# Optimization experiments

Measured on AMD Instinct MI355X. Metric: run time of the kernel, lower is better.

Reference implementation:

```python
import jax, jax.numpy as jnp
import numpy as np
import math

DIM = 1024
N_HEADS = 16
HEAD_DIM = DIM // N_HEADS
FFN_HIDDEN = 4096
EPS = 1e-6


def setup_inputs() -> dict:
    key = jax.random.key(0)
    ks = jax.random.split(key, 10)
    s = 1.0 / math.sqrt(DIM)
    sh = 1.0 / math.sqrt(FFN_HIDDEN)
    return {
        "x": jax.random.normal(ks[0], (2, 2048, DIM), dtype=jnp.float32),
        # attention weights stored as [in, out] (y = x @ W)
        "wq": jax.random.normal(ks[1], (DIM, DIM), dtype=jnp.float32) * s,
        "wk": jax.random.normal(ks[2], (DIM, DIM), dtype=jnp.float32) * s,
        "wv": jax.random.normal(ks[3], (DIM, DIM), dtype=jnp.float32) * s,
        "wo": jax.random.normal(ks[4], (DIM, DIM), dtype=jnp.float32) * s,
        "w_gate": jax.random.normal(ks[5], (DIM, FFN_HIDDEN), dtype=jnp.float32) * s,
        "w_up": jax.random.normal(ks[6], (DIM, FFN_HIDDEN), dtype=jnp.float32) * s,
        "w_down": jax.random.normal(ks[7], (FFN_HIDDEN, DIM), dtype=jnp.float32) * sh,
        "attn_norm_w": jnp.ones((DIM,), dtype=jnp.float32),
        "ffn_norm_w": jnp.ones((DIM,), dtype=jnp.float32),
    }


def rmsnorm(x, w):
    xf = x.astype(jnp.float32)
    rms = jax.lax.rsqrt(jnp.mean(xf * xf, axis=-1, keepdims=True) + EPS)
    return (xf * rms).astype(x.dtype) * w


def attention(x, wq, wk, wv, wo):
    B, T, C = x.shape
    q = (x @ wq).reshape(B, T, N_HEADS, HEAD_DIM)
    k = (x @ wk).reshape(B, T, N_HEADS, HEAD_DIM)
    v = (x @ wv).reshape(B, T, N_HEADS, HEAD_DIM)
    scores = jnp.einsum("bqhd,bkhd->bhqk", q, k) / math.sqrt(HEAD_DIM)
    causal = jnp.tril(jnp.ones((T, T), dtype=bool))  # True = keep
    scores = jnp.where(causal, scores, -jnp.inf)
    attn = jax.nn.softmax(scores, axis=-1)
    out = jnp.einsum("bhqk,bkhd->bqhd", attn, v).reshape(B, T, C)
    return out @ wo


def swiglu(x, w_gate, w_up, w_down):
    return (jax.nn.silu(x @ w_gate) * (x @ w_up)) @ w_down


def reference(x, wq, wk, wv, wo, w_gate, w_up, w_down, attn_norm_w, ffn_norm_w):
    x = x + attention(rmsnorm(x, attn_norm_w), wq, wk, wv, wo)
    x = x + swiglu(rmsnorm(x, ffn_norm_w), w_gate, w_up, w_down)
    return x
```

## Files before the change

kernel.cpp:

```cpp
#include <hip/hip_runtime.h>
#include <hip/hip_bf16.h>
#include <stdint.h>
#include <math.h>

#define DIM   1024
#define TSEQ  2048
#define BATCH 2
#define NH    16
#define HD    64
#define FFN   4096
#define ROWS  (BATCH*TSEQ)
#define QKVN  (3*DIM)

typedef __attribute__((ext_vector_type(8))) short s16x8;
typedef __attribute__((ext_vector_type(4))) float f32x4;

__device__ __forceinline__ unsigned short f2bf(float f) {
  union { float f; unsigned u; } v; v.f = f;
  unsigned r = v.u + 0x7fffu + ((v.u >> 16) & 1u);
  return (unsigned short)(r >> 16);
}
__device__ __forceinline__ float bf2f(unsigned short h) {
  union { unsigned u; float f; } v; v.u = ((unsigned)h) << 16; return v.f;
}
__device__ __forceinline__ unsigned pack_bf2(float lo, float hi) {
  union { float f; unsigned u; } a, c; a.f = lo; c.f = hi;
  return (c.u & 0xffff0000u) | (a.u >> 16);
}

__device__ __forceinline__ void gld16(const void* g, void* l) {
  __builtin_amdgcn_global_load_lds((const __attribute__((address_space(1))) void*)g,
                                   (__attribute__((address_space(3))) void*)l, 16, 0, 0);
}

__device__ __forceinline__ int xcd_swz_flat() {
  const int nx = gridDim.x, ny = gridDim.y;
  const int nwg = nx * ny * gridDim.z;
  const int flat = blockIdx.x + nx * (blockIdx.y + ny * blockIdx.z);
  return (flat & 7) * (nwg >> 3) + (flat >> 3);
}

__global__ void wtrans_k(const float* __restrict__ w, unsigned short* __restrict__ wt,
                         int K, int N, int mode)
{
  __shared__ unsigned short t[64][65];
  const int n0 = blockIdx.x * 64, k0 = blockIdx.y * 64;
  const int tid = threadIdx.x;
  #pragma unroll
  for (int i = 0; i < 16; ++i) {
    const int r = i*4 + (tid >> 6), c = tid & 63;
    t[r][c] = f2bf(w[(size_t)(k0 + r) * N + n0 + c]);
  }
  __syncthreads();
  #pragma unroll
  for (int i = 0; i < 16; ++i) {
    const int r = i*4 + (tid >> 6), c = tid & 63;
    const int n = n0 + r;
    int dr = n;
    if (mode == 1) dr = ((n >> 4) << 5) + (n & 15);
    if (mode == 2) dr = ((n >> 4) << 5) + 16 + (n & 15);
    wt[(size_t)dr * K + k0 + c] = t[c][r];
  }
}

__global__ void vtrans_k(const unsigned short* __restrict__ qkv, unsigned short* __restrict__ vt)
{
  __shared__ unsigned short t[64][65];
  const int tt0 = blockIdx.x * 64;
  const int bh = blockIdx.y, b = bh >> 4, h = bh & 15;
  const int tid = threadIdx.x;
  const unsigned short* src = qkv + (size_t)(b*TSEQ + tt0) * QKVN + 2*DIM + h*HD;
  #pragma unroll
  for (int i = 0; i < 16; ++i) {
    const int r = i*4 + (tid >> 6), c = tid & 63;
    t[r][c] = src[(size_t)r * QKVN + c];
  }
  __syncthreads();
  unsigned short* dst = vt + (size_t)bh * HD * TSEQ + tt0;
  #pragma unroll
  for (int i = 0; i < 16; ++i) {
    const int d = i*4 + (tid >> 6), c = tid & 63;
    dst[(size_t)d * TSEQ + c] = t[c][d];
  }
}

__global__ void rmsnorm_k(const float* __restrict__ x, const float* __restrict__ w,
                          unsigned short* __restrict__ o)
{
  const int row = blockIdx.x, tid = threadIdx.x;
  const float4 v = ((const float4*)(x + (size_t)row * DIM))[tid];
  float ss = v.x*v.x + v.y*v.y + v.z*v.z + v.w*v.w;
  #pragma unroll
  for (int off = 32; off >= 1; off >>= 1) ss += __shfl_xor(ss, off);
  __shared__ float sred[4];
  if ((tid & 63) == 0) sred[tid >> 6] = ss;
  __syncthreads();
  const float tot = sred[0] + sred[1] + sred[2] + sred[3];
  const float r = rsqrtf(tot * (1.0f/DIM) + 1e-6f);
  const float4 wv = ((const float4*)w)[tid];
  ushort4 ov;
  ov.x = f2bf(v.x*r*wv.x); ov.y = f2bf(v.y*r*wv.y);
  ov.z = f2bf(v.z*r*wv.z); ov.w = f2bf(v.w*r*wv.w);
  ((ushort4*)(o + (size_t)row * DIM))[tid] = ov;
}

__global__ void rmsnorm3_k(const float* __restrict__ x, const float* __restrict__ p0,
                           const float* __restrict__ p1, const float* __restrict__ w,
                           float* __restrict__ x1, unsigned short* __restrict__ o)
{
  const int row = blockIdx.x, tid = threadIdx.x;
  const size_t base = (size_t)row * DIM;
  const float4 a = ((const float4*)(x + base))[tid];
  const float4 b = ((const float4*)(p0 + base))[tid];
  const float4 c = ((const float4*)(p1 + base))[tid];
  float4 v;
  v.x = a.x + b.x + c.x; v.y = a.y + b.y + c.y;
  v.z = a.z + b.z + c.z; v.w = a.w + b.w + c.w;
  ((float4*)(x1 + base))[tid] = v;
  float ss = v.x*v.x + v.y*v.y + v.z*v.z + v.w*v.w;
  #pragma unroll
  for (int off = 32; off >= 1; off >>= 1) ss += __shfl_xor(ss, off);
  __shared__ float sred[4];
  if ((tid & 63) == 0) sred[tid >> 6] = ss;
  __syncthreads();
  const float tot = sred[0] + sred[1] + sred[2] + sred[3];
  const float r = rsqrtf(tot * (1.0f/DIM) + 1e-6f);
  const float4 wv = ((const float4*)w)[tid];
  ushort4 ov;
  ov.x = f2bf(v.x*r*wv.x); ov.y = f2bf(v.y*r*wv.y);
  ov.z = f2bf(v.z*r*wv.z); ov.w = f2bf(v.w*r*wv.w);
  ((ushort4*)(o + base))[tid] = ov;
}

__global__ void resadd3_k(const float* __restrict__ x1, const float* __restrict__ q0,
                          const float* __restrict__ q1, float* __restrict__ o)
{
  const size_t i = (size_t)blockIdx.x * 256 + threadIdx.x;
  const float4 a = ((const float4*)x1)[i];
  const float4 b = ((const float4*)q0)[i];
  const float4 c = ((const float4*)q1)[i];
  float4 v;
  v.x = a.x + b.x + c.x; v.y = a.y + b.y + c.y;
  v.z = a.z + b.z + c.z; v.w = a.w + b.w + c.w;
  ((float4*)o)[i] = v;
}

__global__ void gemm128sp(const unsigned short* __restrict__ A, int lda,
                          const unsigned short* __restrict__ BT, int ldb,
                          float* __restrict__ P, int ldc, int Khalf)
{
  __shared__ __align__(16) unsigned short lA[128*64];
  __shared__ __align__(16) unsigned short lB[128*64];
  const int nx = gridDim.x, ny = gridDim.y;
  const int w = xcd_swz_flat();
  const int bx = w % nx, by = (w / nx) % ny, bz = w / (nx * ny);
  const int tid = threadIdx.x;
  const int lane = tid & 63;
  const int wid = tid >> 6;
  const int m0 = by * 128, n0 = bx * 128;
  const int Koff = bz * Khalf;
  P += (size_t)bz * ((size_t)ny * 128) * ldc;
  const int wr = (wid >> 1) * 64, wc = (wid & 1) * 64;
  const int lrow = lane & 15, lk8 = (lane >> 4) * 8;

  f32x4 acc[4][4] = {};

  for (int k0 = Koff; k0 < Koff + Khalf; k0 += 64) {
    #pragma unroll
    for (int c = 0; c < 4; ++c) {
      const int boff = c*4096 + tid*16;
      const int row = boff >> 7, colb = boff & 127;
      gld16((const char*)A + ((size_t)(m0+row)*lda + k0)*2 + colb, (char*)lA + boff);
    }
    #pragma unroll
    for (int c = 0; c < 4; ++c) {
      const int boff = c*4096 + tid*16;
      const int row = boff >> 7, colb = boff & 127;
      gld16((const char*)BT + ((size_t)(n0+row)*ldb + k0)*2 + colb, (char*)lB + boff);
    }
    __syncthreads();
    #pragma unroll
    for (int kk = 0; kk < 64; kk += 32) {
      s16x8 af[4], bf[4];
      #pragma unroll
      for (int i = 0; i < 4; ++i) af[i] = *(const s16x8*)&lA[(wr + i*16 + lrow)*64 + kk + lk8];
      #pragma unroll
      for (int j = 0; j < 4; ++j) bf[j] = *(const s16x8*)&lB[(wc + j*16 + lrow)*64 + kk + lk8];
      #pragma unroll
      for (int i = 0; i < 4; ++i)
        #pragma unroll
        for (int j = 0; j < 4; ++j)
          acc[i][j] = __builtin_amdgcn_mfma_f32_16x16x32_bf16(af[i], bf[j], acc[i][j], 0, 0, 0);
    }
    __syncthreads();
  }
  const int er = (lane >> 4) * 4, ec = lane & 15;
  #pragma unroll
  for (int i = 0; i < 4; ++i)
    #pragma unroll
    for (int j = 0; j < 4; ++j) {
      const int gr = m0 + wr + i*16 + er;
      const int gc = n0 + wc + j*16 + ec;
      #pragma unroll
      for (int e = 0; e < 4; ++e)
        P[(size_t)(gr + e) * ldc + gc] = acc[i][j][e];
    }
}

template<int EPI>
__global__ __launch_bounds__(512) void gemm256(const unsigned short* __restrict__ A, int lda,
                                               const unsigned short* __restrict__ BT, int ldb,
                                               void* __restrict__ Cout, int ldc, int K)
{
  __shared__ __align__(16) unsigned short lA[2][256*64];
  __shared__ __align__(16) unsigned short lB[2][256*64];
  const int nx = gridDim.x;
  const int wsz = xcd_swz_flat();
  const int bx = wsz % nx, by = wsz / nx;
  const int tid = threadIdx.x, lane = tid & 63, wid = tid >> 6;
  const int lrow = lane & 15, g = lane >> 4;
  const int wm = wid >> 2, wn = wid & 3;
  const int m0 = by * 256, n0 = bx * 256;

  const int r0 = tid >> 3;
  const int eB = ((r0 >> 5) << 6) | (r0 & 31);
  const int lc0 = ((tid & 7) * 16) ^ ((r0 & 7) << 4);
  const char* pA = (const char*)A + ((size_t)(m0 + r0) * lda) * 2 + lc0;
  const char* pB = (const char*)BT + ((size_t)(n0 + eB) * ldb) * 2 + lc0;
  char* dA = (char*)&lA[0][0] + tid * 16;
  char* dB = (char*)&lB[0][0] + eB * 128 + (tid & 7) * 16;
  const size_t a64 = (size_t)64 * lda * 2;
  const size_t b32 = (size_t)32 * ldb * 2;

#define STG_GA0(t) do { const char* s_ = pA + (size_t)(t) * 128; \
    char* d_ = dA + (((t) & 1) * 32768); \
    gld16(s_, d_); gld16(s_ + 2*a64, d_ + 16384); } while (0)
#define STG_GA1(t) do { const char* s_ = pA + (size_t)(t) * 128 + a64; \
    char* d_ = dA + (((t) & 1) * 32768) + 8192; \
    gld16(s_, d_); gld16(s_ + 2*a64, d_ + 16384); } while (0)
#define STG_GB0(t) do { const char* s_ = pB + (size_t)(t) * 128; \
    char* d_ = dB + (((t) & 1) * 32768); \
    gld16(s_, d_); gld16(s_ + 4*b32, d_ + 16384); } while (0)
#define STG_GB1(t) do { const char* s_ = pB + (size_t)(t) * 128 + b32; \
    char* d_ = dB + (((t) & 1) * 32768) + 4096; \
    gld16(s_, d_); gld16(s_ + 4*b32, d_ + 16384); } while (0)

  const int swz = (lrow & 7) << 4;
  const int c0 = (g * 16) ^ swz;
  const int c1 = c0 ^ 64;
  const char* rdA = (const char*)&lA[0][0] + (wm * 128 + lrow) * 128;
  const char* rdB = (const char*)&lB[0][0] + (wn * 64 + lrow) * 128;

  f32x4 acc[8][4] = {};
  s16x8 a0[4][2], a1[4][2], b0[2][2], b1[2][2];

#define MFMA_Q(rh, ch, AF, BF) do { \
    _Pragma("unroll") \
    for (int i_ = 0; i_ < 4; ++i_) { \
      _Pragma("unroll") \
      for (int j_ = 0; j_ < 2; ++j_) { \
        acc[(rh)*4+i_][(ch)*2+j_] = __builtin_amdgcn_mfma_f32_16x16x32_bf16(AF[i_][0], BF[j_][0], acc[(rh)*4+i_][(ch)*2+j_], 0,0,0); \
        acc[(rh)*4+i_][(ch)*2+j_] = __builtin_amdgcn_mfma_f32_16x16x32_bf16(AF[i_][1], BF[j_][1], acc[(rh)*4+i_][(ch)*2+j_], 0,0,0); \
      } } } while (0)

  const int NT = K >> 6;

  STG_GA0(0); STG_GB0(0); STG_GB1(0); STG_GA1(0);
  asm volatile("s_waitcnt vmcnt(4)" ::: "memory");
  __builtin_amdgcn_s_barrier();

  for (int t = 0; t < NT; ++t) {
    const char* bufA = rdA + (t & 1) * 32768;
    const char* bufB = rdB + (t & 1) * 32768;
    const bool more = (t + 1 < NT);
    #pragma unroll
    for (int i = 0; i < 4; ++i) {
      a0[i][0] = *(const s16x8*)(bufA + i*2048 + c0);
      a0[i][1] = *(const s16x8*)(bufA + i*2048 + c1);
    }
    #pragma unroll
    for (int j = 0; j < 2; ++j) {
      b0[j][0] = *(const s16x8*)(bufB + j*2048 + c0);
      b0[j][1] = *(const s16x8*)(bufB + j*2048 + c1);
    }
    if (more) { STG_GA0(t + 1); STG_GB0(t + 1); }
    __builtin_amdgcn_s_barrier();
    asm volatile("s_waitcnt lgkmcnt(0)" ::: "memory");
    __builtin_amdgcn_sched_barrier(0);
    __builtin_amdgcn_s_setprio(1);
    MFMA_Q(0, 0, a0, b0);
    __builtin_amdgcn_s_setprio(0);
    if (more) { asm volatile("s_waitcnt vmcnt(6)" ::: "memory"); }
    else      { asm volatile("s_waitcnt vmcnt(2)" ::: "memory"); }
    __builtin_amdgcn_s_barrier();
    #pragma unroll
    for (int j = 0; j < 2; ++j) {
      b1[j][0] = *(const s16x8*)(bufB + 4096 + j*2048 + c0);
      b1[j][1] = *(const s16x8*)(bufB + 4096 + j*2048 + c1);
    }
    if (more) STG_GB1(t + 1);
    __builtin_amdgcn_s_barrier();
    asm volatile("s_waitcnt lgkmcnt(0)" ::: "memory");
    __builtin_amdgcn_sched_barrier(0);
    __builtin_amdgcn_s_setprio(1);
    MFMA_Q(0, 1, a0, b1);
    __builtin_amdgcn_s_setprio(0);
    if (more) { asm volatile("s_waitcnt vmcnt(6)" ::: "memory"); }
    else      { asm volatile("s_waitcnt vmcnt(0)" ::: "memory"); }
    __builtin_amdgcn_s_barrier();
    #pragma unroll
    for (int i = 0; i < 4; ++i) {
      a1[i][0] = *(const s16x8*)(bufA + 8192 + i*2048 + c0);
      a1[i][1] = *(const s16x8*)(bufA + 8192 + i*2048 + c1);
    }
    if (more) STG_GA1(t + 1);
    __builtin_amdgcn_s_barrier();
    asm volatile("s_waitcnt lgkmcnt(0)" ::: "memory");
    __builtin_amdgcn_sched_barrier(0);
    __builtin_amdgcn_s_setprio(1);
    MFMA_Q(1, 1, a1, b1);
    __builtin_amdgcn_s_setprio(0);
    __builtin_amdgcn_s_barrier();
    __builtin_amdgcn_s_setprio(1);
    MFMA_Q(1, 0, a1, b0);
    __builtin_amdgcn_s_setprio(0);
    if (more) { asm volatile("s_waitcnt vmcnt(4)" ::: "memory"); }
    __builtin_amdgcn_s_barrier();
  }

  const int er = g * 4, ec = lane & 15;
  if (EPI == 0) {
    unsigned short* C = (unsigned short*)Cout;
    #pragma unroll
    for (int i = 0; i < 8; ++i)
      #pragma unroll
      for (int j = 0; j < 4; ++j) {
        const int gr = m0 + wm*128 + i*16 + er;
        const int gc = n0 + wn*64 + j*16 + ec;
        #pragma unroll
        for (int e = 0; e < 4; ++e)
          C[(size_t)(gr + e) * ldc + gc] = f2bf(acc[i][j][e]);
      }
  } else {
    unsigned short* C = (unsigned short*)Cout;
    #pragma unroll
    for (int i = 0; i < 8; ++i)
      #pragma unroll
      for (int tp = 0; tp < 2; ++tp) {
        const int gr = m0 + wm*128 + i*16 + er;
        const int hc = (n0 >> 1) + wn*32 + tp*16 + ec;
        #pragma unroll
        for (int e = 0; e < 4; ++e) {
          const float gv = acc[i][2*tp][e];
          const float uv = acc[i][2*tp + 1][e];
          const float hv = gv / (1.f + __expf(-gv)) * uv;
          C[(size_t)(gr + e) * ldc + hc] = f2bf(hv);
        }
      }
  }
#undef STG_GA0
#undef STG_GA1
#undef STG_GB0
#undef STG_GB1
#undef MFMA_Q
}

__global__ __launch_bounds__(512) void attn_fwd(const unsigned short* __restrict__ qkv,
                                                const unsigned short* __restrict__ vt,
                                                unsigned short* __restrict__ outp)
{
  __shared__ __align__(16) unsigned short lK[2][64*64];
  __shared__ __align__(16) unsigned short lV[2][64*64];
  const int nx = gridDim.x;
  const int wsz = xcd_swz_flat();
  const int qblk = wsz % nx;
  const int bh = wsz / nx, b = bh >> 4, h = bh & 15;
  const int tid = threadIdx.x, wid = tid >> 6, lane = tid & 63;
  const int lq = lane & 15, g = lane >> 4;

  const int qrow = qblk*128 + wid*16;
  const int myq = qrow + lq;

  const size_t qbase = ((size_t)(b*TSEQ + myq)) * QKVN + h*HD;
  const s16x8 qf0 = *(const s16x8*)&qkv[qbase + g*8];
  const s16x8 qf1 = *(const s16x8*)&qkv[qbase + 32 + g*8];

  const int boff = tid * 16;
  const int loff = boff ^ (((boff >> 7) & 7) << 4);
  const int srow = loff >> 7;
  const int scolb = loff & 127;
  const char* ksrc0 = (const char*)qkv +
      (((size_t)(b*TSEQ + srow)) * QKVN + DIM + h*HD) * 2 + scolb;
  const char* vsrc0 = (const char*)vt +
      (((size_t)bh*HD + srow) * TSEQ) * 2 + scolb;

  float mrun = -INFINITY, lrun = 0.f;
  f32x4 of[4] = {};

  const int nkt = 2*qblk + 2;

  gld16(ksrc0, (char*)lK[0] + boff);
  gld16(vsrc0, (char*)lV[0] + boff);
  int cur = 0;

  for (int kt = 0; kt < nkt; ++kt) {
    __syncthreads();
    if (kt + 1 < nkt) {
      gld16(ksrc0 + (size_t)(kt+1)*64*(QKVN*2), (char*)lK[cur^1] + boff);
      gld16(vsrc0 + (size_t)(kt+1)*128,         (char*)lV[cur^1] + boff);
    }
    if (kt*64 <= qrow + 15) {
      const unsigned short* Kb = lK[cur];
      const unsigned short* Vb = lV[cur];
      f32x4 sacc[4] = {};
      #pragma unroll
      for (int s = 0; s < 4; ++s) {
        const int r = s*16 + lq;
        const int sw = (r & 7) << 4;
        const s16x8 kf0 = *(const s16x8*)((const char*)Kb + r*128 + ((g*16) ^ sw));
        const s16x8 kf1 = *(const s16x8*)((const char*)Kb + r*128 + ((64 + g*16) ^ sw));
        sacc[s] = __builtin_amdgcn_mfma_f32_16x16x32_bf16(kf0, qf0, sacc[s], 0,0,0);
        sacc[s] = __builtin_amdgcn_mfma_f32_16x16x32_bf16(kf1, qf1, sacc[s], 0,0,0);
      }
      float p[4][4];
      float mt = -INFINITY;
      #pragma unroll
      for (int s = 0; s < 4; ++s)
        #pragma unroll
        for (int e = 0; e < 4; ++e) {
          const int key = kt*64 + s*16 + 4*g + e;
          const float v = (key <= myq) ? sacc[s][e]*0.125f : -INFINITY;
          p[s][e] = v;
          mt = fmaxf(mt, v);
        }
      mt = fmaxf(mt, __shfl_xor(mt, 16));
      mt = fmaxf(mt, __shfl_xor(mt, 32));
      const float mnew = fmaxf(mrun, mt);
      const float scale = __expf(mrun - mnew);
      float ssum = 0.f;
      #pragma unroll
      for (int s = 0; s < 4; ++s)
        #pragma unroll
        for (int e = 0; e < 4; ++e) {
          p[s][e] = __expf(p[s][e] - mnew);
          ssum += p[s][e];
        }
      ssum += __shfl_xor(ssum, 16);
      ssum += __shfl_xor(ssum, 32);
      lrun = lrun * scale + ssum;
      mrun = mnew;
      #pragma unroll
      for (int d0b = 0; d0b < 4; ++d0b) of[d0b] = of[d0b] * scale;
      #pragma unroll
      for (int hh = 0; hh < 2; ++hh) {
        unsigned w[4];
        #pragma unroll
        for (int j = 0; j < 4; ++j) w[j] = pack_bf2(p[2*hh][j], p[2*hh+1][j]);
        s16x8 bp;
        #pragma unroll
        for (int e = 0; e < 8; ++e) {
          const int srcg = 2*(g & 1) + (e >> 2);
          const unsigned ww = (unsigned)__shfl((int)w[e & 3], lq | (srcg << 4));
          bp[e] = (short)((g >= 2) ? (ww >> 16) : (ww & 0xffffu));
        }
        #pragma unroll
        for (int d0b = 0; d0b < 4; ++d0b) {
          const int r = d0b*16 + lq;
          const int sw = (r & 7) << 4;
          const s16x8 vf = *(const s16x8*)((const char*)Vb + r*128 + ((hh*64 + g*16) ^ sw));
          of[d0b] = __builtin_amdgcn_mfma_f32_16x16x32_bf16(vf, bp, of[d0b], 0,0,0);
        }
      }
    }
    cur ^= 1;
  }
  const float inv = 1.f / lrun;
  const size_t obase = ((size_t)(b*TSEQ + myq)) * DIM + h*HD;
  #pragma unroll
  for (int d0b = 0; d0b < 4; ++d0b) {
    ushort4 o;
    o.x = f2bf(of[d0b][0] * inv);
    o.y = f2bf(of[d0b][1] * inv);
    o.z = f2bf(of[d0b][2] * inv);
    o.w = f2bf(of[d0b][3] * inv);
    *(ushort4*)&outp[obase + d0b*16 + 4*g] = o;
  }
}

extern "C" void kernel_launch(void* const* d_in, const int* in_sizes, int n_in,
                              void* d_out, int out_size, void* d_ws, size_t ws_size,
                              hipStream_t stream)
{
  const float* x   = (const float*)d_in[0];
  const float* wq  = (const float*)d_in[1];
  const float* wk  = (const float*)d_in[2];
  const float* wv  = (const float*)d_in[3];
  const float* wo  = (const float*)d_in[4];
  const float* wg  = (const float*)d_in[5];
  const float* wu  = (const float*)d_in[6];
  const float* wd  = (const float*)d_in[7];
  const float* anw = (const float*)d_in[8];
  const float* fnw = (const float*)d_in[9];
  float* outp = (float*)d_out;

  const size_t MB = 1024*1024;
  char* ws = (char*)d_ws;
  float*          x1    = (float*)         (ws + 0);
  unsigned short* wdT   = (unsigned short*)(ws + 16*MB);
  unsigned short* wguT  = (unsigned short*)(ws + 24*MB);
  unsigned short* wqkvT = (unsigned short*)(ws + 40*MB);
  unsigned short* woT   = (unsigned short*)(ws + 46*MB);
  unsigned short* xn    = (unsigned short*)(ws + 48*MB);
  unsigned short* qkv   = (unsigned short*)(ws + 56*MB);
  unsigned short* vtb   = (unsigned short*)(ws + 80*MB);
  unsigned short* aout  = (unsigned short*)(ws + 88*MB);
  float*          pwo   = (float*)         (ws + 56*MB);
  unsigned short* hbuf  = (unsigned short*)(ws + 56*MB);
  float*          pdn   = (float*)         (ws + 24*MB);

  const dim3 blk(256);

  wtrans_k<<<dim3(16,16), blk, 0, stream>>>(wq, wqkvT,               DIM, DIM, 0);
  wtrans_k<<<dim3(16,16), blk, 0, stream>>>(wk, wqkvT + 1024*1024,   DIM, DIM, 0);
  wtrans_k<<<dim3(16,16), blk, 0, stream>>>(wv, wqkvT + 2*1024*1024, DIM, DIM, 0);
  wtrans_k<<<dim3(16,16), blk, 0, stream>>>(wo, woT,                 DIM, DIM, 0);
  wtrans_k<<<dim3(64,16), blk, 0, stream>>>(wg, wguT,                DIM, FFN, 1);
  wtrans_k<<<dim3(64,16), blk, 0, stream>>>(wu, wguT,                DIM, FFN, 2);
  wtrans_k<<<dim3(16,64), blk, 0, stream>>>(wd, wdT,                 FFN, DIM, 0);

  rmsnorm_k<<<ROWS, blk, 0, stream>>>(x, anw, xn);
  gemm256<0><<<dim3(QKVN/256, ROWS/256), dim3(512), 0, stream>>>(xn, DIM, wqkvT, DIM, qkv, QKVN, DIM);
  vtrans_k<<<dim3(TSEQ/64, BATCH*NH), blk, 0, stream>>>(qkv, vtb);
  attn_fwd<<<dim3(TSEQ/128, BATCH*NH), dim3(512), 0, stream>>>(qkv, vtb, aout);
  gemm128sp<<<dim3(DIM/128, ROWS/128, 2), blk, 0, stream>>>(aout, DIM, woT, DIM, pwo, DIM, DIM/2);
  rmsnorm3_k<<<ROWS, blk, 0, stream>>>(x, pwo, pwo + (size_t)ROWS*DIM, fnw, x1, xn);

  gemm256<2><<<dim3(2*FFN/256, ROWS/256), dim3(512), 0, stream>>>(xn, DIM, wguT, DIM, hbuf, FFN, DIM);
  gemm128sp<<<dim3(DIM/128, ROWS/128, 2), blk, 0, stream>>>(hbuf, FFN, wdT, FFN, pdn, DIM, FFN/2);
  resadd3_k<<<dim3(ROWS*DIM/1024), blk, 0, stream>>>(x1, pdn, pdn + (size_t)ROWS*DIM, outp);
}
```

Before: 321.7 us.

## Peel last GEMM iteration, reorder prefetch before LDS reads, merge QKV transposes

The gemm256 main loop is restructured so the final k-tile is peeled out, which removes the per-iteration `more` branches. Global prefetch stores are now issued before the LDS fragment reads, and several barriers are dropped (the ones that came before lgkmcnt waits). Separately, the three Q/K/V weight transpose launches are merged into one 3D-grid kernel to cut launch overhead. The reduced barrier set risks LDS write/read hazards if the double-buffer waits are not sufficient.

```diff
diff --git a/kernel.cpp b/kernel.cpp
--- a/kernel.cpp
+++ b/kernel.cpp
@@ -60,6 +60,27 @@
     if (mode == 1) dr = ((n >> 4) << 5) + (n & 15);
     if (mode == 2) dr = ((n >> 4) << 5) + 16 + (n & 15);
     wt[(size_t)dr * K + k0 + c] = t[c][r];
+  }
+}
+
+__global__ void wtrans_qkv_k(const float* __restrict__ wq, const float* __restrict__ wk,
+                             const float* __restrict__ wv, unsigned short* __restrict__ wt)
+{
+  __shared__ unsigned short t[64][65];
+  const int n0 = blockIdx.x * 64, k0 = blockIdx.y * 64, z = blockIdx.z;
+  const float* w = (z == 0) ? wq : (z == 1) ? wk : wv;
+  unsigned short* dst = wt + (size_t)z * DIM * DIM;
+  const int tid = threadIdx.x;
+  #pragma unroll
+  for (int i = 0; i < 16; ++i) {
+    const int r = i*4 + (tid >> 6), c = tid & 63;
+    t[r][c] = f2bf(w[(size_t)(k0 + r) * DIM + n0 + c]);
+  }
+  __syncthreads();
+  #pragma unroll
+  for (int i = 0; i < 16; ++i) {
+    const int r = i*4 + (tid >> 6), c = tid & 63;
+    dst[(size_t)(n0 + r) * DIM + k0 + c] = t[c][r];
   }
 }
 
@@ -263,69 +284,71 @@
         acc[(rh)*4+i_][(ch)*2+j_] = __builtin_amdgcn_mfma_f32_16x16x32_bf16(AF[i_][1], BF[j_][1], acc[(rh)*4+i_][(ch)*2+j_], 0,0,0); \
       } } } while (0)
 
+#define VMCNT(n) asm volatile("s_waitcnt vmcnt(" #n ")" ::: "memory")
+#define LGKM0()  do { asm volatile("s_waitcnt lgkmcnt(0)" ::: "memory"); \
+                      __builtin_amdgcn_sched_barrier(0); } while (0)
+#define BARRIER() do { __builtin_amdgcn_s_barrier(); \
+                       __builtin_amdgcn_sched_barrier(0); } while (0)
+
+#define DS_A0(buf) do { _Pragma("unroll") for (int i_ = 0; i_ < 4; ++i_) { \
+    a0[i_][0] = *(const s16x8*)((buf) + i_*2048 + c0); \
+    a0[i_][1] = *(const s16x8*)((buf) + i_*2048 + c1); } } while (0)
+#define DS_A1(buf) do { _Pragma("unroll") for (int i_ = 0; i_ < 4; ++i_) { \
+    a1[i_][0] = *(const s16x8*)((buf) + 8192 + i_*2048 + c0); \
+    a1[i_][1] = *(const s16x8*)((buf) + 8192 + i_*2048 + c1); } } while (0)
+#define DS_B0(buf) do { _Pragma("unroll") for (int j_ = 0; j_ < 2; ++j_) { \
+    b0[j_][0] = *(const s16x8*)((buf) + j_*2048 + c0); \
+    b0[j_][1] = *(const s16x8*)((buf) + j_*2048 + c1); } } while (0)
+#define DS_B1(buf) do { _Pragma("unroll") for (int j_ = 0; j_ < 2; ++j_) { \
+    b1[j_][0] = *(const s16x8*)((buf) + 4096 + j_*2048 + c0); \
+    b1[j_][1] = *(const s16x8*)((buf) + 4096 + j_*2048 + c1); } } while (0)
+
+#define PRIO_MFMA(rh, ch, AF, BF) do { \
+    __builtin_amdgcn_s_setprio(1); MFMA_Q(rh, ch, AF, BF); \
+    __builtin_amdgcn_s_setprio(0); } while (0)
+
   const int NT = K >> 6;
 
   STG_GA0(0); STG_GB0(0); STG_GB1(0); STG_GA1(0);
-  asm volatile("s_waitcnt vmcnt(4)" ::: "memory");
-  __builtin_amdgcn_s_barrier();
-
-  for (int t = 0; t < NT; ++t) {
+  VMCNT(4);
+  BARRIER();
+
+  for (int t = 0; t < NT - 1; ++t) {
     const char* bufA = rdA + (t & 1) * 32768;
     const char* bufB = rdB + (t & 1) * 32768;
-    const bool more = (t + 1 < NT);
-    #pragma unroll
-    for (int i = 0; i < 4; ++i) {
-      a0[i][0] = *(const s16x8*)(bufA + i*2048 + c0);
-      a0[i][1] = *(const s16x8*)(bufA + i*2048 + c1);
-    }
-    #pragma unroll
-    for (int j = 0; j < 2; ++j) {
-      b0[j][0] = *(const s16x8*)(bufB + j*2048 + c0);
-      b0[j][1] = *(const s16x8*)(bufB + j*2048 + c1);
-    }
-    if (more) { STG_GA0(t + 1); STG_GB0(t + 1); }
-    __builtin_amdgcn_s_barrier();
-    asm volatile("s_waitcnt lgkmcnt(0)" ::: "memory");
-    __builtin_amdgcn_sched_barrier(0);
-    __builtin_amdgcn_s_setprio(1);
-    MFMA_Q(0, 0, a0, b0);
-    __builtin_amdgcn_s_setprio(0);
-    if (more) { asm volatile("s_waitcnt vmcnt(6)" ::: "memory"); }
-    else      { asm volatile("s_waitcnt vmcnt(2)" ::: "memory"); }
-    __builtin_amdgcn_s_barrier();
-    #pragma unroll
-    for (int j = 0; j < 2; ++j) {
-      b1[j][0] = *(const s16x8*)(bufB + 4096 + j*2048 + c0);
-      b1[j][1] = *(const s16x8*)(bufB + 4096 + j*2048 + c1);
-    }
-    if (more) STG_GB1(t + 1);
-    __builtin_amdgcn_s_barrier();
-    asm volatile("s_waitcnt lgkmcnt(0)" ::: "memory");
-    __builtin_amdgcn_sched_barrier(0);
-    __builtin_amdgcn_s_setprio(1);
-    MFMA_Q(0, 1, a0, b1);
-    __builtin_amdgcn_s_setprio(0);
-    if (more) { asm volatile("s_waitcnt vmcnt(6)" ::: "memory"); }
-    else      { asm volatile("s_waitcnt vmcnt(0)" ::: "memory"); }
-    __builtin_amdgcn_s_barrier();
-    #pragma unroll
-    for (int i = 0; i < 4; ++i) {
-      a1[i][0] = *(const s16x8*)(bufA + 8192 + i*2048 + c0);
-      a1[i][1] = *(const s16x8*)(bufA + 8192 + i*2048 + c1);
-    }
-    if (more) STG_GA1(t + 1);
-    __builtin_amdgcn_s_barrier();
-    asm volatile("s_waitcnt lgkmcnt(0)" ::: "memory");
-    __builtin_amdgcn_sched_barrier(0);
-    __builtin_amdgcn_s_setprio(1);
-    MFMA_Q(1, 1, a1, b1);
-    __builtin_amdgcn_s_setprio(0);
-    __builtin_amdgcn_s_barrier();
-    __builtin_amdgcn_s_setprio(1);
-    MFMA_Q(1, 0, a1, b0);
-    __builtin_amdgcn_s_setprio(0);
-    if (more) { asm volatile("s_waitcnt vmcnt(4)" ::: "memory"); }
-    __builtin_amdgcn_s_barrier();
+    STG_GA0(t + 1); STG_GB0(t + 1);
+    DS_A0(bufA); DS_B0(bufB);
+    LGKM0();
+    PRIO_MFMA(0, 0, a0, b0);
+    VMCNT(6); BARRIER();
+    STG_GB1(t + 1);
+    DS_B1(bufB);
+    LGKM0();
+    PRIO_MFMA(0, 1, a0, b1);
+    VMCNT(6); BARRIER();
+    STG_GA1(t + 1);
+    DS_A1(bufA);
+    LGKM0();
+    PRIO_MFMA(1, 1, a1, b1);
+    BARRIER();
+    PRIO_MFMA(1, 0, a1, b0);
+    VMCNT(4); BARRIER();
+  }
+  {
+    const char* bufA = rdA + ((NT - 1) & 1) * 32768;
+    const char* bufB = rdB + ((NT - 1) & 1) * 32768;
+    DS_A0(bufA); DS_B0(bufB);
+    LGKM0();
+    PRIO_MFMA(0, 0, a0, b0);
+    VMCNT(2); BARRIER();
+    DS_B1(bufB);
+    LGKM0();
+    PRIO_MFMA(0, 1, a0, b1);
+    VMCNT(0); BARRIER();
+    DS_A1(bufA);
+    LGKM0();
+    PRIO_MFMA(1, 1, a1, b1);
+    PRIO_MFMA(1, 0, a1, b0);
   }
 
   const int er = g * 4, ec = lane & 15;
@@ -363,6 +386,14 @@
 #undef STG_GB0
 #undef STG_GB1
 #undef MFMA_Q
+#undef VMCNT
+#undef LGKM0
+#undef BARRIER
+#undef DS_A0
+#undef DS_A1
+#undef DS_B0
+#undef DS_B1
+#undef PRIO_MFMA
 }
 
 __global__ __launch_bounds__(512) void attn_fwd(const unsigned short* __restrict__ qkv,
@@ -520,13 +551,11 @@
 
   const dim3 blk(256);
 
-  wtrans_k<<<dim3(16,16), blk, 0, stream>>>(wq, wqkvT,               DIM, DIM, 0);
-  wtrans_k<<<dim3(16,16), blk, 0, stream>>>(wk, wqkvT + 1024*1024,   DIM, DIM, 0);
-  wtrans_k<<<dim3(16,16), blk, 0, stream>>>(wv, wqkvT + 2*1024*1024, DIM, DIM, 0);
-  wtrans_k<<<dim3(16,16), blk, 0, stream>>>(wo, woT,                 DIM, DIM, 0);
-  wtrans_k<<<dim3(64,16), blk, 0, stream>>>(wg, wguT,                DIM, FFN, 1);
-  wtrans_k<<<dim3(64,16), blk, 0, stream>>>(wu, wguT,                DIM, FFN, 2);
-  wtrans_k<<<dim3(16,64), blk, 0, stream>>>(wd, wdT,                 FFN, DIM, 0);
+  wtrans_qkv_k<<<dim3(16,16,3), blk, 0, stream>>>(wq, wk, wv, wqkvT);
+  wtrans_k<<<dim3(16,16), blk, 0, stream>>>(wo, woT, DIM, DIM, 0);
+  wtrans_k<<<dim3(64,16), blk, 0, stream>>>(wg, wguT, DIM, FFN, 1);
+  wtrans_k<<<dim3(64,16), blk, 0, stream>>>(wu, wguT, DIM, FFN, 2);
+  wtrans_k<<<dim3(16,64), blk, 0, stream>>>(wd, wdT, FFN, DIM, 0);
 
   rmsnorm_k<<<ROWS, blk, 0, stream>>>(x, anw, xn);
   gemm256<0><<<dim3(QKVN/256, ROWS/256), dim3(512), 0, stream>>>(xn, DIM, wqkvT, DIM, qkv, QKVN, DIM);
```

Result: slower. 347.6 us (+8.1%).

## Store split-K partials in bf16, split down-proj 4-way, and cluster GEMM tiles per XCD

Applied to the files above, without the earlier changes.

The split-K GEMM partial outputs are now written as bf16 instead of fp32, which halves partial-sum write and read traffic in the residual and norm kernels. The down projection is split four ways along K instead of two, for more parallelism, and the final residual kernel sums four partials. gemm256 maps tiles to XCDs as rectangular clusters to improve L2 reuse, and the three QKV weight transposes are merged into one launch. Rounding the partials to bf16 adds numerical error to the residual stream.

```diff
diff --git a/kernel.cpp b/kernel.cpp
--- a/kernel.cpp
+++ b/kernel.cpp
@@ -60,6 +60,27 @@
     if (mode == 1) dr = ((n >> 4) << 5) + (n & 15);
     if (mode == 2) dr = ((n >> 4) << 5) + 16 + (n & 15);
     wt[(size_t)dr * K + k0 + c] = t[c][r];
+  }
+}
+
+__global__ void wtrans_qkv_k(const float* __restrict__ wq, const float* __restrict__ wk,
+                             const float* __restrict__ wv, unsigned short* __restrict__ wt)
+{
+  __shared__ unsigned short t[64][65];
+  const int n0 = blockIdx.x * 64, k0 = blockIdx.y * 64, z = blockIdx.z;
+  const float* w = (z == 0) ? wq : (z == 1) ? wk : wv;
+  unsigned short* dst = wt + (size_t)z * DIM * DIM;
+  const int tid = threadIdx.x;
+  #pragma unroll
+  for (int i = 0; i < 16; ++i) {
+    const int r = i*4 + (tid >> 6), c = tid & 63;
+    t[r][c] = f2bf(w[(size_t)(k0 + r) * DIM + n0 + c]);
+  }
+  __syncthreads();
+  #pragma unroll
+  for (int i = 0; i < 16; ++i) {
+    const int r = i*4 + (tid >> 6), c = tid & 63;
+    dst[(size_t)(n0 + r) * DIM + k0 + c] = t[c][r];
   }
 }
 
@@ -104,18 +125,18 @@
   ((ushort4*)(o + (size_t)row * DIM))[tid] = ov;
 }
 
-__global__ void rmsnorm3_k(const float* __restrict__ x, const float* __restrict__ p0,
-                           const float* __restrict__ p1, const float* __restrict__ w,
+__global__ void rmsnorm3_k(const float* __restrict__ x, const unsigned short* __restrict__ p0,
+                           const unsigned short* __restrict__ p1, const float* __restrict__ w,
                            float* __restrict__ x1, unsigned short* __restrict__ o)
 {
   const int row = blockIdx.x, tid = threadIdx.x;
   const size_t base = (size_t)row * DIM;
   const float4 a = ((const float4*)(x + base))[tid];
-  const float4 b = ((const float4*)(p0 + base))[tid];
-  const float4 c = ((const float4*)(p1 + base))[tid];
+  const ushort4 b = ((const ushort4*)(p0 + base))[tid];
+  const ushort4 c = ((const ushort4*)(p1 + base))[tid];
   float4 v;
-  v.x = a.x + b.x + c.x; v.y = a.y + b.y + c.y;
-  v.z = a.z + b.z + c.z; v.w = a.w + b.w + c.w;
+  v.x = a.x + bf2f(b.x) + bf2f(c.x); v.y = a.y + bf2f(b.y) + bf2f(c.y);
+  v.z = a.z + bf2f(b.z) + bf2f(c.z); v.w = a.w + bf2f(b.w) + bf2f(c.w);
   ((float4*)(x1 + base))[tid] = v;
   float ss = v.x*v.x + v.y*v.y + v.z*v.z + v.w*v.w;
   #pragma unroll
@@ -132,22 +153,29 @@
   ((ushort4*)(o + base))[tid] = ov;
 }
 
-__global__ void resadd3_k(const float* __restrict__ x1, const float* __restrict__ q0,
-                          const float* __restrict__ q1, float* __restrict__ o)
+__global__ void resadd5_k(const float* __restrict__ x1,
+                          const unsigned short* __restrict__ q0, const unsigned short* __restrict__ q1,
+                          const unsigned short* __restrict__ q2, const unsigned short* __restrict__ q3,
+                          float* __restrict__ o)
 {
   const size_t i = (size_t)blockIdx.x * 256 + threadIdx.x;
   const float4 a = ((const float4*)x1)[i];
-  const float4 b = ((const float4*)q0)[i];
-  const float4 c = ((const float4*)q1)[i];
+  const ushort4 b = ((const ushort4*)q0)[i];
+  const ushort4 c = ((const ushort4*)q1)[i];
+  const ushort4 d = ((const ushort4*)q2)[i];
+  const ushort4 e = ((const ushort4*)q3)[i];
   float4 v;
-  v.x = a.x + b.x + c.x; v.y = a.y + b.y + c.y;
-  v.z = a.z + b.z + c.z; v.w = a.w + b.w + c.w;
+  v.x = a.x + bf2f(b.x) + bf2f(c.x) + bf2f(d.x) + bf2f(e.x);
+  v.y = a.y + bf2f(b.y) + bf2f(c.y) + bf2f(d.y) + bf2f(e.y);
+  v.z = a.z + bf2f(b.z) + bf2f(c.z) + bf2f(d.z) + bf2f(e.z);
+  v.w = a.w + bf2f(b.w) + bf2f(c.w) + bf2f(d.w) + bf2f(e.w);
   ((float4*)o)[i] = v;
 }
 
+template<int NS>
 __global__ void gemm128sp(const unsigned short* __restrict__ A, int lda,
                           const unsigned short* __restrict__ BT, int ldb,
-                          float* __restrict__ P, int ldc, int Khalf)
+                          unsigned short* __restrict__ P, int ldc, int Ksp)
 {
   __shared__ __align__(16) unsigned short lA[128*64];
   __shared__ __align__(16) unsigned short lB[128*64];
@@ -158,14 +186,14 @@
   const int lane = tid & 63;
   const int wid = tid >> 6;
   const int m0 = by * 128, n0 = bx * 128;
-  const int Koff = bz * Khalf;
+  const int Koff = bz * Ksp;
   P += (size_t)bz * ((size_t)ny * 128) * ldc;
   const int wr = (wid >> 1) * 64, wc = (wid & 1) * 64;
   const int lrow = lane & 15, lk8 = (lane >> 4) * 8;
 
   f32x4 acc[4][4] = {};
 
-  for (int k0 = Koff; k0 < Koff + Khalf; k0 += 64) {
+  for (int k0 = Koff; k0 < Koff + Ksp; k0 += 64) {
     #pragma unroll
     for (int c = 0; c < 4; ++c) {
       const int boff = c*4096 + tid*16;
@@ -203,20 +231,25 @@
       const int gc = n0 + wc + j*16 + ec;
       #pragma unroll
       for (int e = 0; e < 4; ++e)
-        P[(size_t)(gr + e) * ldc + gc] = acc[i][j][e];
+        P[(size_t)(gr + e) * ldc + gc] = f2bf(acc[i][j][e]);
     }
 }
 
 template<int EPI>
 __global__ __launch_bounds__(512) void gemm256(const unsigned short* __restrict__ A, int lda,
                                                const unsigned short* __restrict__ BT, int ldb,
-                                               void* __restrict__ Cout, int ldc, int K)
+                                               void* __restrict__ Cout, int ldc, int K,
+                                               int CX, int CY)
 {
   __shared__ __align__(16) unsigned short lA[2][256*64];
   __shared__ __align__(16) unsigned short lB[2][256*64];
-  const int nx = gridDim.x;
-  const int wsz = xcd_swz_flat();
-  const int bx = wsz % nx, by = wsz / nx;
+  const int nx = gridDim.x, ny = gridDim.y;
+  const int flat = blockIdx.x + nx * blockIdx.y;
+  const int xcd = flat & 7, k = flat >> 3;
+  const int RX = nx / CX, RY = ny / CY;
+  const int cx = xcd % CX, cy = xcd / CX;
+  const int bx = cx * RX + k % RX;
+  const int by = cy * RY + k / RX;
   const int tid = threadIdx.x, lane = tid & 63, wid = tid >> 6;
   const int lrow = lane & 15, g = lane >> 4;
   const int wm = wid >> 2, wn = wid & 3;
@@ -504,6 +537,7 @@
   float* outp = (float*)d_out;
 
   const size_t MB = 1024*1024;
+  const size_t RD = (size_t)ROWS * DIM;
   char* ws = (char*)d_ws;
   float*          x1    = (float*)         (ws + 0);
   unsigned short* wdT   = (unsigned short*)(ws + 16*MB);
@@ -514,28 +548,26 @@
   unsigned short* qkv   = (unsigned short*)(ws + 56*MB);
   unsigned short* vtb   = (unsigned short*)(ws + 80*MB);
   unsigned short* aout  = (unsigned short*)(ws + 88*MB);
-  float*          pwo   = (float*)         (ws + 56*MB);
+  unsigned short* pwo   = (unsigned short*)(ws + 56*MB);
   unsigned short* hbuf  = (unsigned short*)(ws + 56*MB);
-  float*          pdn   = (float*)         (ws + 24*MB);
+  unsigned short* pdn   = (unsigned short*)(ws + 24*MB);
 
   const dim3 blk(256);
 
-  wtrans_k<<<dim3(16,16), blk, 0, stream>>>(wq, wqkvT,               DIM, DIM, 0);
-  wtrans_k<<<dim3(16,16), blk, 0, stream>>>(wk, wqkvT + 1024*1024,   DIM, DIM, 0);
-  wtrans_k<<<dim3(16,16), blk, 0, stream>>>(wv, wqkvT + 2*1024*1024, DIM, DIM, 0);
-  wtrans_k<<<dim3(16,16), blk, 0, stream>>>(wo, woT,                 DIM, DIM, 0);
-  wtrans_k<<<dim3(64,16), blk, 0, stream>>>(wg, wguT,                DIM, FFN, 1);
-  wtrans_k<<<dim3(64,16), blk, 0, stream>>>(wu, wguT,                DIM, FFN, 2);
-  wtrans_k<<<dim3(16,64), blk, 0, stream>>>(wd, wdT,                 FFN, DIM, 0);
+  wtrans_qkv_k<<<dim3(16,16,3), blk, 0, stream>>>(wq, wk, wv, wqkvT);
+  wtrans_k<<<dim3(16,16), blk, 0, stream>>>(wo, woT, DIM, DIM, 0);
+  wtrans_k<<<dim3(64,16), blk, 0, stream>>>(wg, wguT, DIM, FFN, 1);
+  wtrans_k<<<dim3(64,16), blk, 0, stream>>>(wu, wguT, DIM, FFN, 2);
+  wtrans_k<<<dim3(16,64), blk, 0, stream>>>(wd, wdT, FFN, DIM, 0);
 
   rmsnorm_k<<<ROWS, blk, 0, stream>>>(x, anw, xn);
-  gemm256<0><<<dim3(QKVN/256, ROWS/256), dim3(512), 0, stream>>>(xn, DIM, wqkvT, DIM, qkv, QKVN, DIM);
+  gemm256<0><<<dim3(QKVN/256, ROWS/256), dim3(512), 0, stream>>>(xn, DIM, wqkvT, DIM, qkv, QKVN, DIM, 4, 2);
   vtrans_k<<<dim3(TSEQ/64, BATCH*NH), blk, 0, stream>>>(qkv, vtb);
   attn_fwd<<<dim3(TSEQ/128, BATCH*NH), dim3(512), 0, stream>>>(qkv, vtb, aout);
-  gemm128sp<<<dim3(DIM/128, ROWS/128, 2), blk, 0, stream>>>(aout, DIM, woT, DIM, pwo, DIM, DIM/2);
-  rmsnorm3_k<<<ROWS, blk, 0, stream>>>(x, pwo, pwo + (size_t)ROWS*DIM, fnw, x1, xn);
-
-  gemm256<2><<<dim3(2*FFN/256, ROWS/256), dim3(512), 0, stream>>>(xn, DIM, wguT, DIM, hbuf, FFN, DIM);
-  gemm128sp<<<dim3(DIM/128, ROWS/128, 2), blk, 0, stream>>>(hbuf, FFN, wdT, FFN, pdn, DIM, FFN/2);
-  resadd3_k<<<dim3(ROWS*DIM/1024), blk, 0, stream>>>(x1, pdn, pdn + (size_t)ROWS*DIM, outp);
-}
+  gemm128sp<2><<<dim3(DIM/128, ROWS/128, 2), blk, 0, stream>>>(aout, DIM, woT, DIM, pwo, DIM, DIM/2);
+  rmsnorm3_k<<<ROWS, blk, 0, stream>>>(x, pwo, pwo + RD, fnw, x1, xn);
+
+  gemm256<2><<<dim3(2*FFN/256, ROWS/256), dim3(512), 0, stream>>>(xn, DIM, wguT, DIM, hbuf, FFN, DIM, 4, 2);
+  gemm128sp<4><<<dim3(DIM/128, ROWS/128, 4), blk, 0, stream>>>(hbuf, FFN, wdT, FFN, pdn, DIM, FFN/4);
+  resadd5_k<<<dim3(ROWS*DIM/1024), blk, 0, stream>>>(x1, pdn, pdn + RD, pdn + 2*RD, pdn + 3*RD, outp);
+}
```

Measured after the change: 299.9 us. 1.07x faster.
